# Kernel tuning notes

Measured on AMD Instinct MI355X. Metric: run time of the kernel, lower is better.

## Reference

```python
import jax, jax.numpy as jnp
import numpy as np

N = 80000        # nodes
E = 1280000      # edges
NG = 8           # graphs (segment ids)
F_IN = 3
NC = 20
BN_EPS = 1e-3    # keras BatchNormalization default epsilon


def setup_inputs() -> dict:
    key = jax.random.key(0)
    ks = jax.random.split(key, 16)
    inp = {}
    inp['x'] = jax.random.normal(ks[0], (N, F_IN), dtype=jnp.float32)
    inp['edge_w'] = jax.random.uniform(ks[1], (E,), dtype=jnp.float32)
    inp['src'] = jax.random.randint(ks[2], (E,), 0, N, dtype=jnp.int32)
    inp['dst'] = jax.random.randint(ks[3], (E,), 0, N, dtype=jnp.int32)
    inp['ids'] = jnp.sort(jax.random.randint(ks[4], (N,), 0, NG, dtype=jnp.int32))
    def w(k, fi, fo):
        return jax.random.normal(k, (fi, fo), dtype=jnp.float32) * (1.0 / np.sqrt(fi))
    inp['W1'] = w(ks[5], F_IN, 32); inp['b1'] = jnp.zeros((32,), jnp.float32)
    inp['W2'] = w(ks[6], 32, 32);   inp['b2'] = jnp.zeros((32,), jnp.float32)
    inp['g1'] = jnp.ones((32,), jnp.float32); inp['be1'] = jnp.zeros((32,), jnp.float32)
    inp['m1'] = jax.random.normal(ks[7], (32,), dtype=jnp.float32) * 0.1
    inp['v1'] = jax.random.uniform(ks[8], (32,), dtype=jnp.float32) + 0.5
    inp['W3'] = w(ks[9], 32, 64);   inp['b3'] = jnp.zeros((64,), jnp.float32)
    inp['W4'] = w(ks[10], 64, 64);  inp['b4'] = jnp.zeros((64,), jnp.float32)
    inp['g2'] = jnp.ones((64,), jnp.float32); inp['be2'] = jnp.zeros((64,), jnp.float32)
    inp['m2'] = jax.random.normal(ks[11], (64,), dtype=jnp.float32) * 0.1
    inp['v2'] = jax.random.uniform(ks[12], (64,), dtype=jnp.float32) + 0.5
    inp['W5'] = w(ks[13], 64, NC);  inp['b5'] = jnp.zeros((NC,), jnp.float32)
    return inp


def _gcn(x, W, b, src, dst, ew):
    # Spektral GCNConv: A_norm @ (X W) + b, with A given as edge list (src->dst).
    h = x @ W                                      # [N, Fo] dense transform first (cheaper)
    msg = h[src] * ew[:, None]                     # gather + scale  [E, Fo]
    agg = jax.ops.segment_sum(msg, dst, num_segments=N)  # scatter-add [N, Fo]
    return agg + b


def _bn(x, g, be, m, v):
    # inference-mode BatchNormalization
    return (x - m) * (g * jax.lax.rsqrt(v + BN_EPS)) + be


def _pool(x, ids):
    # per-graph global max pooling, broadcast back to nodes
    mx = jax.ops.segment_max(x, ids, num_segments=NG)   # [NG, F]
    return mx[ids]                                       # [N, F]


def reference(x, edge_w, src, dst, ids,
              W1, b1, W2, b2, g1, be1, m1, v1,
              W3, b3, W4, b4, g2, be2, m2, v2,
              W5, b5):
    h = jax.nn.relu(_gcn(x, W1, b1, src, dst, edge_w))
    h = jax.nn.relu(_gcn(h, W2, b2, src, dst, edge_w))
    h = _bn(h, g1, be1, m1, v1)
    h = _pool(h, ids)
    h = jax.nn.relu(_gcn(h, W3, b3, src, dst, edge_w))
    h = jax.nn.relu(_gcn(h, W4, b4, src, dst, edge_w))
    h = _bn(h, g2, be2, m2, v2)
    h = _pool(h, ids)
    # dropout is identity in inference
    out = jax.nn.softmax(_gcn(h, W5, b5, src, dst, edge_w), axis=-1)
    return out
```

## Files before the change

kernel.cpp:

```cpp
#include <hip/hip_runtime.h>

#define NN 80000
#define NE 1280000
#define NGR 8
#define BN_EPS 1e-3f
#define NBF 625
#define GB 1280
#define CHK 1000

typedef unsigned short ushort;
typedef __attribute__((ext_vector_type(8))) short bf16x8;
typedef __attribute__((ext_vector_type(4))) float f32x4;

__device__ __forceinline__ unsigned enc_f(float f) {
    unsigned b = __float_as_uint(f);
    return (f >= 0.f) ? (b | 0x80000000u) : ~b;
}
__device__ __forceinline__ float dec_f(unsigned u) {
    return (u & 0x80000000u) ? __uint_as_float(u & 0x7FFFFFFFu) : __uint_as_float(~u);
}
__device__ __forceinline__ ushort f2bf(float f) {
    unsigned u = __float_as_uint(f);
    unsigned r = u + 0x7FFFu + ((u >> 16) & 1u);
    return (ushort)(r >> 16);
}
__device__ __forceinline__ void fma8(float* acc, const ushort* p, float w) {
    uint4 q = *(const uint4*)p;
    acc[0] += w * __uint_as_float((q.x & 0xFFFFu) << 16);
    acc[1] += w * __uint_as_float(q.x & 0xFFFF0000u);
    acc[2] += w * __uint_as_float((q.y & 0xFFFFu) << 16);
    acc[3] += w * __uint_as_float(q.y & 0xFFFF0000u);
    acc[4] += w * __uint_as_float((q.z & 0xFFFFu) << 16);
    acc[5] += w * __uint_as_float(q.z & 0xFFFF0000u);
    acc[6] += w * __uint_as_float((q.w & 0xFFFFu) << 16);
    acc[7] += w * __uint_as_float(q.w & 0xFFFF0000u);
}

__global__ __launch_bounds__(256) void k_bhist(const int* __restrict__ dst,
                                               int* __restrict__ hcnt) {
    __shared__ int lh[NBF];
    for (int i = threadIdx.x; i < NBF; i += 256) lh[i] = 0;
    __syncthreads();
    int e0 = blockIdx.x * CHK;
    for (int e = e0 + threadIdx.x; e < e0 + CHK; e += 256)
        atomicAdd(&lh[dst[e] >> 7], 1);
    __syncthreads();
    int* row = hcnt + (size_t)blockIdx.x * NBF;
    for (int i = threadIdx.x; i < NBF; i += 256) row[i] = lh[i];
}

__global__ __launch_bounds__(256) void k_bbase1(int* __restrict__ hcnt,
                                                int* __restrict__ tot) {
    __shared__ int sm[256];
    int bin = blockIdx.x, t = threadIdx.x;
    int v[5];
    int s = 0;
    #pragma unroll
    for (int j = 0; j < 5; ++j) {
        v[j] = hcnt[(size_t)(t * 5 + j) * NBF + bin];
        s += v[j];
    }
    sm[t] = s;
    __syncthreads();
    #pragma unroll
    for (int off = 1; off < 256; off <<= 1) {
        int u = (t >= off) ? sm[t - off] : 0;
        __syncthreads();
        sm[t] += u;
        __syncthreads();
    }
    int run = sm[t] - s;
    if (t == 255) tot[bin] = sm[255];
    #pragma unroll
    for (int j = 0; j < 5; ++j) {
        hcnt[(size_t)(t * 5 + j) * NBF + bin] = run;
        run += v[j];
    }
}

__global__ __launch_bounds__(1024) void k_bbase2(const int* __restrict__ tot,
                                                 int* __restrict__ bo) {
    __shared__ int sm[1024];
    int t = threadIdx.x;
    int v = (t < NBF) ? tot[t] : 0;
    sm[t] = v;
    __syncthreads();
    #pragma unroll
    for (int off = 1; off < 1024; off <<= 1) {
        int u = (t >= off) ? sm[t - off] : 0;
        __syncthreads();
        sm[t] += u;
        __syncthreads();
    }
    if (t < NBF) bo[t] = sm[t] - v;
    if (t == 0) bo[NBF] = NE;
}

__global__ __launch_bounds__(256) void k_bfill(const int* __restrict__ src,
                                               const int* __restrict__ dst,
                                               const float* __restrict__ ew,
                                               const int* __restrict__ ids,
                                               const int* __restrict__ hcnt,
                                               const int* __restrict__ bo,
                                               int2* __restrict__ cB) {
    __shared__ int lcur[NBF];
    const int* row = hcnt + (size_t)blockIdx.x * NBF;
    for (int i = threadIdx.x; i < NBF; i += 256) lcur[i] = row[i] + bo[i];
    __syncthreads();
    int e0 = blockIdx.x * CHK;
    for (int e = e0 + threadIdx.x; e < e0 + CHK; e += 256) {
        int d = dst[e];
        int s = src[e];
        int pos = atomicAdd(&lcur[d >> 7], 1);
        cB[pos] = make_int2(s | (ids[s] << 17) | ((d & 127) << 20),
                            __float_as_int(ew[e]));
    }
}

__global__ __launch_bounds__(512) void k_insort(const int* __restrict__ bo,
                                                const int2* __restrict__ cB,
                                                int* __restrict__ rp,
                                                int2* __restrict__ cE) {
    __shared__ int lc[128];
    __shared__ int loff[128];
    __shared__ int sm[512];
    int bin = blockIdx.x, t = threadIdx.x;
    int s0 = bo[bin], s1 = bo[bin + 1];
    if (t < 128) lc[t] = 0;
    __syncthreads();
    for (int i = s0 + t; i < s1; i += 512)
        atomicAdd(&lc[(cB[i].x >> 20) & 127], 1);
    __syncthreads();
    int v = (t < 128) ? lc[t] : 0;
    sm[t] = v;
    __syncthreads();
    #pragma unroll
    for (int off = 1; off < 128; off <<= 1) {
        int u = (t >= off && t < 128) ? sm[t - off] : 0;
        __syncthreads();
        if (t < 128) sm[t] += u;
        __syncthreads();
    }
    if (t < 128) {
        loff[t] = sm[t] - v;
        rp[bin * 128 + t] = s0 + loff[t];
        lc[t] = 0;
    }
    if (bin == NBF - 1 && t == 0) rp[NN] = NE;
    __syncthreads();
    for (int i = s0 + t; i < s1; i += 512) {
        int2 a = cB[i];
        int dlow = (a.x >> 20) & 127;
        int pos = s0 + loff[dlow] + atomicAdd(&lc[dlow], 1);
        cE[pos] = make_int2((a.x & 0x1FFFF) | (((a.x >> 17) & 7) << 24), a.y);
    }
}

__global__ __launch_bounds__(256) void k_wprep(const float* __restrict__ W2,
                                               const float* __restrict__ W4,
                                               ushort* __restrict__ W2t,
                                               ushort* __restrict__ W4t) {
    int t = threadIdx.x;
    for (int i = t; i < 32 * 32; i += 256) {
        int f = i >> 5, k = i & 31;
        W2t[i] = f2bf(W2[k * 32 + f]);
    }
    for (int i = t; i < 64 * 64; i += 256) {
        int f = i >> 6, k = i & 63;
        W4t[i] = f2bf(W4[k * 64 + f]);
    }
}

__global__ __launch_bounds__(256) void k_gSX(const float* __restrict__ x,
                                             const int* __restrict__ rp,
                                             const int2* __restrict__ cE,
                                             float* __restrict__ S,
                                             float* __restrict__ AX) {
    int n = blockIdx.x * 256 + threadIdx.x;
    if (n >= NN) return;
    int e0 = rp[n], e1 = rp[n + 1];
    float sv[8] = {0, 0, 0, 0, 0, 0, 0, 0};
    float ax0 = 0.f, ax1 = 0.f, ax2 = 0.f;
    for (int i = e0; i < e1; ++i) {
        int2 a = cE[i];
        float w = __int_as_float(a.y);
        int s = a.x & 0xFFFFFF;
        int gg = a.x >> 24;
        #pragma unroll
        for (int g = 0; g < 8; ++g) sv[g] += (gg == g) ? w : 0.f;
        const float* xp = x + s * 3;
        ax0 += w * xp[0]; ax1 += w * xp[1]; ax2 += w * xp[2];
    }
    float4* Sp = (float4*)(S + n * 8);
    Sp[0] = make_float4(sv[0], sv[1], sv[2], sv[3]);
    Sp[1] = make_float4(sv[4], sv[5], sv[6], sv[7]);
    *(float4*)(AX + n * 4) = make_float4(ax0, ax1, ax2, 0.f);
}

__global__ __launch_bounds__(256) void k_l12m(const float* __restrict__ AX,
                                              const float* __restrict__ W1,
                                              const float* __restrict__ b1,
                                              const ushort* __restrict__ W2t,
                                              ushort* __restrict__ T) {
    __shared__ ushort h1s[64 * 40];
    int t = threadIdx.x;
    int nb = blockIdx.x * 64;
    {
        int f = t & 31, rr = t >> 5;
        float w0 = W1[f], w1 = W1[32 + f], w2 = W1[64 + f], bb = b1[f];
        #pragma unroll
        for (int i = 0; i < 8; ++i) {
            int n = rr + i * 8;
            float4 ax = *(const float4*)(AX + (nb + n) * 4);
            float acc = bb + ax.x * w0 + ax.y * w1 + ax.z * w2;
            h1s[n * 40 + f] = f2bf(fmaxf(acc, 0.f));
        }
    }
    __syncthreads();
    int lane = t & 63, wave = t >> 6;
    int quad = lane >> 4, col = lane & 15;
    int mtile = wave;
    bf16x8 a = *(const bf16x8*)(h1s + (mtile * 16 + col) * 40 + quad * 8);
    #pragma unroll
    for (int ntile = 0; ntile < 2; ++ntile) {
        bf16x8 b = *(const bf16x8*)(W2t + (ntile * 16 + col) * 32 + quad * 8);
        f32x4 acc = {0.f, 0.f, 0.f, 0.f};
        acc = __builtin_amdgcn_mfma_f32_16x16x32_bf16(a, b, acc, 0, 0, 0);
        #pragma unroll
        for (int r = 0; r < 4; ++r) {
            int node = nb + mtile * 16 + quad * 4 + r;
            T[node * 32 + ntile * 16 + col] = f2bf(acc[r]);
        }
    }
}

__global__ __launch_bounds__(256) void k_l34m(const float* __restrict__ S,
                                              const float* __restrict__ HW3,
                                              const float* __restrict__ b3,
                                              const ushort* __restrict__ W4t,
                                              ushort* __restrict__ T) {
    __shared__ ushort h3s[64 * 72];
    int t = threadIdx.x;
    int nb = blockIdx.x * 64;
    {
        int f = t & 63, rr = t >> 6;
        float hwc[8];
        #pragma unroll
        for (int g = 0; g < 8; ++g) hwc[g] = HW3[g * 64 + f];
        float bb = b3[f];
        #pragma unroll
        for (int i = 0; i < 16; ++i) {
            int n = rr + i * 4;
            const float4* sp = (const float4*)(S + (size_t)(nb + n) * 8);
            float4 s0 = sp[0], s1 = sp[1];
            float acc = bb + s0.x * hwc[0] + s0.y * hwc[1] + s0.z * hwc[2] +
                        s0.w * hwc[3] + s1.x * hwc[4] + s1.y * hwc[5] +
                        s1.z * hwc[6] + s1.w * hwc[7];
            h3s[n * 72 + f] = f2bf(fmaxf(acc, 0.f));
        }
    }
    __syncthreads();
    int lane = t & 63, wave = t >> 6;
    int quad = lane >> 4, col = lane & 15;
    int mtile = wave;
    bf16x8 a0 = *(const bf16x8*)(h3s + (mtile * 16 + col) * 72 + quad * 8);
    bf16x8 a1 = *(const bf16x8*)(h3s + (mtile * 16 + col) * 72 + 32 + quad * 8);
    #pragma unroll
    for (int ntile = 0; ntile < 4; ++ntile) {
        bf16x8 b0 = *(const bf16x8*)(W4t + (ntile * 16 + col) * 64 + quad * 8);
        bf16x8 b1v = *(const bf16x8*)(W4t + (ntile * 16 + col) * 64 + 32 + quad * 8);
        f32x4 acc = {0.f, 0.f, 0.f, 0.f};
        acc = __builtin_amdgcn_mfma_f32_16x16x32_bf16(a0, b0, acc, 0, 0, 0);
        acc = __builtin_amdgcn_mfma_f32_16x16x32_bf16(a1, b1v, acc, 0, 0, 0);
        #pragma unroll
        for (int r = 0; r < 4; ++r) {
            int node = nb + mtile * 16 + quad * 4 + r;
            T[node * 64 + ntile * 16 + col] = f2bf(acc[r]);
        }
    }
}

template <int LOGF>
__global__ __launch_bounds__(256) void k_gpool(const ushort* __restrict__ th,
                                               const int* __restrict__ rp,
                                               const int2* __restrict__ cE,
                                               const int* __restrict__ ids,
                                               const float* __restrict__ b,
                                               const float* __restrict__ g,
                                               const float* __restrict__ be,
                                               const float* __restrict__ m,
                                               const float* __restrict__ v,
                                               unsigned* __restrict__ mxe) {
    const int F = 1 << LOGF;
    const int CPN = F >> 3;
    const int NPB = 256 / CPN;
    __shared__ unsigned lmx[NGR * F];
    for (int i = threadIdx.x; i < NGR * F; i += 256) lmx[i] = 0u;
    __syncthreads();
    int c = threadIdx.x & (CPN - 1);
    int n = blockIdx.x * NPB + (threadIdx.x >> (LOGF - 3));
    if (n < NN) {
        int e0 = rp[n], e1 = rp[n + 1];
        float acc[8] = {0, 0, 0, 0, 0, 0, 0, 0};
        float acc2[8] = {0, 0, 0, 0, 0, 0, 0, 0};
        int i = e0;
        for (; i + 2 <= e1; i += 2) {
            int2 a0 = cE[i], a1 = cE[i + 1];
            const ushort* p0 = th + (((size_t)(a0.x & 0xFFFFFF)) << LOGF) + (c << 3);
            const ushort* p1 = th + (((size_t)(a1.x & 0xFFFFFF)) << LOGF) + (c << 3);
            fma8(acc, p0, __int_as_float(a0.y));
            fma8(acc2, p1, __int_as_float(a1.y));
        }
        if (i < e1) {
            int2 a0 = cE[i];
            fma8(acc, th + (((size_t)(a0.x & 0xFFFFFF)) << LOGF) + (c << 3),
                 __int_as_float(a0.y));
        }
        int gg = ids[n];
        #pragma unroll
        for (int j = 0; j < 8; ++j) {
            int f = (c << 3) + j;
            float scale = g[f] * rsqrtf(v[f] + BN_EPS);
            float h = fmaxf(acc[j] + acc2[j] + b[f], 0.f);
            float val = (h - m[f]) * scale + be[f];
            atomicMax(&lmx[gg * F + f], enc_f(val));
        }
    }
    __syncthreads();
    for (int i = threadIdx.x; i < NGR * F; i += 256) {
        unsigned u = lmx[i];
        if (u) atomicMax(&mxe[i], u);
    }
}

__global__ __launch_bounds__(512) void k_dechw3(const unsigned* __restrict__ mxe,
                                                const float* __restrict__ W,
                                                float* __restrict__ HW) {
    __shared__ float smx[256];
    int t = threadIdx.x;
    if (t < 256) smx[t] = mxe[t] ? dec_f(mxe[t]) : 0.f;
    __syncthreads();
    int g = t >> 6, f = t & 63;
    float acc = 0.f;
    #pragma unroll
    for (int k = 0; k < 32; ++k) acc += smx[g * 32 + k] * W[k * 64 + f];
    HW[t] = acc;
}

__global__ __launch_bounds__(512) void k_dechw5(const unsigned* __restrict__ mxe,
                                                const float* __restrict__ W,
                                                float* __restrict__ HW) {
    __shared__ float smx[512];
    int t = threadIdx.x;
    smx[t] = mxe[t] ? dec_f(mxe[t]) : 0.f;
    __syncthreads();
    if (t >= 160) return;
    int g = t / 20, c = t % 20;
    float acc = 0.f;
    #pragma unroll
    for (int k = 0; k < 64; ++k) acc += smx[g * 64 + k] * W[k * 20 + c];
    HW[t] = acc;
}

__global__ __launch_bounds__(256) void k_out(const float* __restrict__ S,
                                             const float* __restrict__ HW5,
                                             const float* __restrict__ b5,
                                             float* __restrict__ out) {
    __shared__ float hw[160];
    __shared__ float bb[20];
    int t = threadIdx.x;
    if (t < 160) hw[t] = HW5[t];
    if (t < 20) bb[t] = b5[t];
    __syncthreads();
    int n = blockIdx.x * 256 + t;
    if (n >= NN) return;
    const float4* sp = (const float4*)(S + n * 8);
    float4 s0 = sp[0], s1 = sp[1];
    float sv[8] = {s0.x, s0.y, s0.z, s0.w, s1.x, s1.y, s1.z, s1.w};
    float pre[20];
    #pragma unroll
    for (int c = 0; c < 20; ++c) {
        float acc = bb[c];
        #pragma unroll
        for (int g = 0; g < 8; ++g) acc += sv[g] * hw[g * 20 + c];
        pre[c] = acc;
    }
    float mx = pre[0];
    #pragma unroll
    for (int c = 1; c < 20; ++c) mx = fmaxf(mx, pre[c]);
    float sum = 0.f;
    #pragma unroll
    for (int c = 0; c < 20; ++c) { pre[c] = __expf(pre[c] - mx); sum += pre[c]; }
    float inv = 1.f / sum;
    #pragma unroll
    for (int c = 0; c < 20; ++c) out[n * 20 + c] = pre[c] * inv;
}

extern "C" void kernel_launch(void* const* d_in, const int* in_sizes, int n_in,
                              void* d_out, int out_size, void* d_ws, size_t ws_size,
                              hipStream_t stream) {
    const float* x   = (const float*)d_in[0];
    const float* ew  = (const float*)d_in[1];
    const int*   src = (const int*)d_in[2];
    const int*   dst = (const int*)d_in[3];
    const int*   ids = (const int*)d_in[4];
    const float* W1 = (const float*)d_in[5];  const float* b1 = (const float*)d_in[6];
    const float* W2 = (const float*)d_in[7];  const float* b2 = (const float*)d_in[8];
    const float* g1 = (const float*)d_in[9];  const float* be1 = (const float*)d_in[10];
    const float* m1 = (const float*)d_in[11]; const float* v1 = (const float*)d_in[12];
    const float* W3 = (const float*)d_in[13]; const float* b3 = (const float*)d_in[14];
    const float* W4 = (const float*)d_in[15]; const float* b4 = (const float*)d_in[16];
    const float* g2 = (const float*)d_in[17]; const float* be2 = (const float*)d_in[18];
    const float* m2 = (const float*)d_in[19]; const float* v2 = (const float*)d_in[20];
    const float* W5 = (const float*)d_in[21]; const float* b5 = (const float*)d_in[22];
    float* out = (float*)d_out;

    char* p = (char*)d_ws;
    float*  S    = (float*)p;  p += (size_t)NN * 8 * 4;
    ushort* T    = (ushort*)p; p += (size_t)NN * 64 * 2;
    float*  AX   = (float*)p;  p += (size_t)NN * 4 * 4;
    int*    rp   = (int*)p;    p += (size_t)(NN + 16) * 4;
    int*    hcnt = (int*)p;    p += (size_t)GB * NBF * 4;
    int*    tot  = (int*)p;    p += 1024 * 4;
    int*    bo   = (int*)p;    p += 1024 * 4;
    int2*   cB   = (int2*)p;   p += (size_t)NE * 8;
    int2*   cE   = (int2*)p;   p += (size_t)NE * 8;
    unsigned* MXE1 = (unsigned*)p; p += 256 * 4;
    unsigned* MXE2 = (unsigned*)p; p += 512 * 4;
    float*  HW3  = (float*)p;  p += 512 * 4;
    float*  HW5  = (float*)p;  p += 256 * 4;
    ushort* W2t  = (ushort*)p; p += 1024 * 2;
    ushort* W4t  = (ushort*)p; p += 4096 * 2;

    const int BS = 256;
    const int gN = (NN + BS - 1) / BS;

    hipMemsetAsync(MXE1, 0, 768 * 4, stream);
    hipLaunchKernelGGL(k_wprep, dim3(1), dim3(BS), 0, stream, W2, W4, W2t, W4t);
    hipLaunchKernelGGL(k_bhist, dim3(GB), dim3(BS), 0, stream, dst, hcnt);
    hipLaunchKernelGGL(k_bbase1, dim3(NBF), dim3(BS), 0, stream, hcnt, tot);
    hipLaunchKernelGGL(k_bbase2, dim3(1), dim3(1024), 0, stream, tot, bo);
    hipLaunchKernelGGL(k_bfill, dim3(GB), dim3(BS), 0, stream, src, dst, ew, ids, hcnt, bo, cB);
    hipLaunchKernelGGL(k_insort, dim3(NBF), dim3(512), 0, stream, bo, cB, rp, cE);

    hipLaunchKernelGGL(k_gSX, dim3(gN), dim3(BS), 0, stream, x, rp, cE, S, AX);

    hipLaunchKernelGGL(k_l12m, dim3(NN / 64), dim3(BS), 0, stream, AX, W1, b1, W2t, T);
    hipLaunchKernelGGL(k_gpool<5>, dim3(NN / 64), dim3(BS), 0, stream, T, rp, cE, ids, b2, g1, be1, m1, v1, MXE1);

    hipLaunchKernelGGL(k_dechw3, dim3(1), dim3(512), 0, stream, MXE1, W3, HW3);
    hipLaunchKernelGGL(k_l34m, dim3(NN / 64), dim3(BS), 0, stream, S, HW3, b3, W4t, T);
    hipLaunchKernelGGL(k_gpool<6>, dim3(NN / 32), dim3(BS), 0, stream, T, rp, cE, ids, b4, g2, be2, m2, v2, MXE2);

    hipLaunchKernelGGL(k_dechw5, dim3(1), dim3(512), 0, stream, MXE2, W5, HW5);
    hipLaunchKernelGGL(k_out, dim3(gN), dim3(BS), 0, stream, S, HW5, b5, out);
}
```

Measured before the change: 274.1 us.

## Fuse small prep kernels into neighbors and widen gather unrolling

Folds the weight-transpose prep into the bin-base scan kernel, fuses the per-node S/AX gather into the insertion-sort kernel (4 threads per node with shuffle reductions), and recomputes the pooled-max times W3/W5 products redundantly inside each block of the consuming kernels. This removes four kernel launches and the extra pass reading cE for S/AX. The gpool gather loop is unrolled to four independent accumulators to raise memory-level parallelism. In exchange, every block of k_l34m and k_out repeats a small matvec.

```diff
diff --git a/kernel.cpp b/kernel.cpp
--- a/kernel.cpp
+++ b/kernel.cpp
@@ -78,8 +78,12 @@
     }
 }
 
-__global__ __launch_bounds__(1024) void k_bbase2(const int* __restrict__ tot,
-                                                 int* __restrict__ bo) {
+__global__ __launch_bounds__(1024) void k_bbase2w(const int* __restrict__ tot,
+                                                  int* __restrict__ bo,
+                                                  const float* __restrict__ W2,
+                                                  const float* __restrict__ W4,
+                                                  ushort* __restrict__ W2t,
+                                                  ushort* __restrict__ W4t) {
     __shared__ int sm[1024];
     int t = threadIdx.x;
     int v = (t < NBF) ? tot[t] : 0;
@@ -94,6 +98,16 @@
     }
     if (t < NBF) bo[t] = sm[t] - v;
     if (t == 0) bo[NBF] = NE;
+    {
+        int f = t >> 5, k = t & 31;
+        W2t[t] = f2bf(W2[k * 32 + f]);
+    }
+    #pragma unroll
+    for (int j = 0; j < 4; ++j) {
+        int i = t + j * 1024;
+        int f = i >> 6, k = i & 63;
+        W4t[i] = f2bf(W4[k * 64 + f]);
+    }
 }
 
 __global__ __launch_bounds__(256) void k_bfill(const int* __restrict__ src,
@@ -119,8 +133,11 @@
 
 __global__ __launch_bounds__(512) void k_insort(const int* __restrict__ bo,
                                                 const int2* __restrict__ cB,
+                                                const float* __restrict__ x,
                                                 int* __restrict__ rp,
-                                                int2* __restrict__ cE) {
+                                                int2* __restrict__ cE,
+                                                float* __restrict__ S,
+                                                float* __restrict__ AX) {
     __shared__ int lc[128];
     __shared__ int loff[128];
     __shared__ int sm[512];
@@ -154,34 +171,13 @@
         int pos = s0 + loff[dlow] + atomicAdd(&lc[dlow], 1);
         cE[pos] = make_int2((a.x & 0x1FFFF) | (((a.x >> 17) & 7) << 24), a.y);
     }
-}
-
-__global__ __launch_bounds__(256) void k_wprep(const float* __restrict__ W2,
-                                               const float* __restrict__ W4,
-                                               ushort* __restrict__ W2t,
-                                               ushort* __restrict__ W4t) {
-    int t = threadIdx.x;
-    for (int i = t; i < 32 * 32; i += 256) {
-        int f = i >> 5, k = i & 31;
-        W2t[i] = f2bf(W2[k * 32 + f]);
-    }
-    for (int i = t; i < 64 * 64; i += 256) {
-        int f = i >> 6, k = i & 63;
-        W4t[i] = f2bf(W4[k * 64 + f]);
-    }
-}
-
-__global__ __launch_bounds__(256) void k_gSX(const float* __restrict__ x,
-                                             const int* __restrict__ rp,
-                                             const int2* __restrict__ cE,
-                                             float* __restrict__ S,
-                                             float* __restrict__ AX) {
-    int n = blockIdx.x * 256 + threadIdx.x;
-    if (n >= NN) return;
-    int e0 = rp[n], e1 = rp[n + 1];
+    __syncthreads();
+    int n = t >> 2, q = t & 3;
+    int ne0 = s0 + loff[n];
+    int ne1 = ne0 + lc[n];
     float sv[8] = {0, 0, 0, 0, 0, 0, 0, 0};
     float ax0 = 0.f, ax1 = 0.f, ax2 = 0.f;
-    for (int i = e0; i < e1; ++i) {
+    for (int i = ne0 + q; i < ne1; i += 4) {
         int2 a = cE[i];
         float w = __int_as_float(a.y);
         int s = a.x & 0xFFFFFF;
@@ -191,10 +187,21 @@
         const float* xp = x + s * 3;
         ax0 += w * xp[0]; ax1 += w * xp[1]; ax2 += w * xp[2];
     }
-    float4* Sp = (float4*)(S + n * 8);
-    Sp[0] = make_float4(sv[0], sv[1], sv[2], sv[3]);
-    Sp[1] = make_float4(sv[4], sv[5], sv[6], sv[7]);
-    *(float4*)(AX + n * 4) = make_float4(ax0, ax1, ax2, 0.f);
+    #pragma unroll
+    for (int g = 0; g < 8; ++g) {
+        sv[g] += __shfl_xor(sv[g], 1);
+        sv[g] += __shfl_xor(sv[g], 2);
+    }
+    ax0 += __shfl_xor(ax0, 1); ax0 += __shfl_xor(ax0, 2);
+    ax1 += __shfl_xor(ax1, 1); ax1 += __shfl_xor(ax1, 2);
+    ax2 += __shfl_xor(ax2, 1); ax2 += __shfl_xor(ax2, 2);
+    if (q == 0) {
+        int node = bin * 128 + n;
+        float4* Sp = (float4*)(S + (size_t)node * 8);
+        Sp[0] = make_float4(sv[0], sv[1], sv[2], sv[3]);
+        Sp[1] = make_float4(sv[4], sv[5], sv[6], sv[7]);
+        *(float4*)(AX + (size_t)node * 4) = make_float4(ax0, ax1, ax2, 0.f);
+    }
 }
 
 __global__ __launch_bounds__(256) void k_l12m(const float* __restrict__ AX,
@@ -235,18 +242,35 @@
 }
 
 __global__ __launch_bounds__(256) void k_l34m(const float* __restrict__ S,
-                                              const float* __restrict__ HW3,
+                                              const unsigned* __restrict__ mxe,
+                                              const float* __restrict__ W3,
                                               const float* __restrict__ b3,
                                               const ushort* __restrict__ W4t,
                                               ushort* __restrict__ T) {
+    __shared__ float smxs[256];
+    __shared__ float HW3s[512];
     __shared__ ushort h3s[64 * 72];
     int t = threadIdx.x;
     int nb = blockIdx.x * 64;
+    smxs[t] = mxe[t] ? dec_f(mxe[t]) : 0.f;
+    __syncthreads();
+    {
+        #pragma unroll
+        for (int j = 0; j < 2; ++j) {
+            int i = t + j * 256;
+            int g = i >> 6, f = i & 63;
+            float acc = 0.f;
+            #pragma unroll
+            for (int k = 0; k < 32; ++k) acc += smxs[g * 32 + k] * W3[k * 64 + f];
+            HW3s[i] = acc;
+        }
+    }
+    __syncthreads();
     {
         int f = t & 63, rr = t >> 6;
         float hwc[8];
         #pragma unroll
-        for (int g = 0; g < 8; ++g) hwc[g] = HW3[g * 64 + f];
+        for (int g = 0; g < 8; ++g) hwc[g] = HW3s[g * 64 + f];
         float bb = b3[f];
         #pragma unroll
         for (int i = 0; i < 16; ++i) {
@@ -301,27 +325,28 @@
     int n = blockIdx.x * NPB + (threadIdx.x >> (LOGF - 3));
     if (n < NN) {
         int e0 = rp[n], e1 = rp[n + 1];
-        float acc[8] = {0, 0, 0, 0, 0, 0, 0, 0};
-        float acc2[8] = {0, 0, 0, 0, 0, 0, 0, 0};
+        float a0[8] = {0, 0, 0, 0, 0, 0, 0, 0};
+        float a1[8] = {0, 0, 0, 0, 0, 0, 0, 0};
+        float a2[8] = {0, 0, 0, 0, 0, 0, 0, 0};
+        float a3[8] = {0, 0, 0, 0, 0, 0, 0, 0};
         int i = e0;
-        for (; i + 2 <= e1; i += 2) {
-            int2 a0 = cE[i], a1 = cE[i + 1];
-            const ushort* p0 = th + (((size_t)(a0.x & 0xFFFFFF)) << LOGF) + (c << 3);
-            const ushort* p1 = th + (((size_t)(a1.x & 0xFFFFFF)) << LOGF) + (c << 3);
-            fma8(acc, p0, __int_as_float(a0.y));
-            fma8(acc2, p1, __int_as_float(a1.y));
-        }
-        if (i < e1) {
-            int2 a0 = cE[i];
-            fma8(acc, th + (((size_t)(a0.x & 0xFFFFFF)) << LOGF) + (c << 3),
-                 __int_as_float(a0.y));
+        for (; i + 4 <= e1; i += 4) {
+            int2 q0 = cE[i], q1 = cE[i + 1], q2 = cE[i + 2], q3 = cE[i + 3];
+            fma8(a0, th + (((size_t)(q0.x & 0xFFFFFF)) << LOGF) + (c << 3), __int_as_float(q0.y));
+            fma8(a1, th + (((size_t)(q1.x & 0xFFFFFF)) << LOGF) + (c << 3), __int_as_float(q1.y));
+            fma8(a2, th + (((size_t)(q2.x & 0xFFFFFF)) << LOGF) + (c << 3), __int_as_float(q2.y));
+            fma8(a3, th + (((size_t)(q3.x & 0xFFFFFF)) << LOGF) + (c << 3), __int_as_float(q3.y));
+        }
+        for (; i < e1; ++i) {
+            int2 q0 = cE[i];
+            fma8(a0, th + (((size_t)(q0.x & 0xFFFFFF)) << LOGF) + (c << 3), __int_as_float(q0.y));
         }
         int gg = ids[n];
         #pragma unroll
         for (int j = 0; j < 8; ++j) {
             int f = (c << 3) + j;
             float scale = g[f] * rsqrtf(v[f] + BN_EPS);
-            float h = fmaxf(acc[j] + acc2[j] + b[f], 0.f);
+            float h = fmaxf((a0[j] + a1[j]) + (a2[j] + a3[j]) + b[f], 0.f);
             float val = (h - m[f]) * scale + be[f];
             atomicMax(&lmx[gg * F + f], enc_f(val));
         }
@@ -333,48 +358,30 @@
     }
 }
 
-__global__ __launch_bounds__(512) void k_dechw3(const unsigned* __restrict__ mxe,
-                                                const float* __restrict__ W,
-                                                float* __restrict__ HW) {
-    __shared__ float smx[256];
-    int t = threadIdx.x;
-    if (t < 256) smx[t] = mxe[t] ? dec_f(mxe[t]) : 0.f;
-    __syncthreads();
-    int g = t >> 6, f = t & 63;
-    float acc = 0.f;
-    #pragma unroll
-    for (int k = 0; k < 32; ++k) acc += smx[g * 32 + k] * W[k * 64 + f];
-    HW[t] = acc;
-}
-
-__global__ __launch_bounds__(512) void k_dechw5(const unsigned* __restrict__ mxe,
-                                                const float* __restrict__ W,
-                                                float* __restrict__ HW) {
-    __shared__ float smx[512];
-    int t = threadIdx.x;
-    smx[t] = mxe[t] ? dec_f(mxe[t]) : 0.f;
-    __syncthreads();
-    if (t >= 160) return;
-    int g = t / 20, c = t % 20;
-    float acc = 0.f;
-    #pragma unroll
-    for (int k = 0; k < 64; ++k) acc += smx[g * 64 + k] * W[k * 20 + c];
-    HW[t] = acc;
-}
-
 __global__ __launch_bounds__(256) void k_out(const float* __restrict__ S,
-                                             const float* __restrict__ HW5,
+                                             const unsigned* __restrict__ mxe,
+                                             const float* __restrict__ W5,
                                              const float* __restrict__ b5,
                                              float* __restrict__ out) {
+    __shared__ float smxs[512];
     __shared__ float hw[160];
     __shared__ float bb[20];
     int t = threadIdx.x;
-    if (t < 160) hw[t] = HW5[t];
+    smxs[t] = mxe[t] ? dec_f(mxe[t]) : 0.f;
+    smxs[t + 256] = mxe[t + 256] ? dec_f(mxe[t + 256]) : 0.f;
     if (t < 20) bb[t] = b5[t];
+    __syncthreads();
+    if (t < 160) {
+        int g = t / 20, c = t % 20;
+        float acc = 0.f;
+        #pragma unroll
+        for (int k = 0; k < 64; ++k) acc += smxs[g * 64 + k] * W5[k * 20 + c];
+        hw[t] = acc;
+    }
     __syncthreads();
     int n = blockIdx.x * 256 + t;
     if (n >= NN) return;
-    const float4* sp = (const float4*)(S + n * 8);
+    const float4* sp = (const float4*)(S + (size_t)n * 8);
     float4 s0 = sp[0], s1 = sp[1];
     float sv[8] = {s0.x, s0.y, s0.z, s0.w, s1.x, s1.y, s1.z, s1.w};
     float pre[20];
@@ -427,8 +434,6 @@
     int2*   cE   = (int2*)p;   p += (size_t)NE * 8;
     unsigned* MXE1 = (unsigned*)p; p += 256 * 4;
     unsigned* MXE2 = (unsigned*)p; p += 512 * 4;
-    float*  HW3  = (float*)p;  p += 512 * 4;
-    float*  HW5  = (float*)p;  p += 256 * 4;
     ushort* W2t  = (ushort*)p; p += 1024 * 2;
     ushort* W4t  = (ushort*)p; p += 4096 * 2;
 
@@ -436,22 +441,17 @@
     const int gN = (NN + BS - 1) / BS;
 
     hipMemsetAsync(MXE1, 0, 768 * 4, stream);
-    hipLaunchKernelGGL(k_wprep, dim3(1), dim3(BS), 0, stream, W2, W4, W2t, W4t);
     hipLaunchKernelGGL(k_bhist, dim3(GB), dim3(BS), 0, stream, dst, hcnt);
     hipLaunchKernelGGL(k_bbase1, dim3(NBF), dim3(BS), 0, stream, hcnt, tot);
-    hipLaunchKernelGGL(k_bbase2, dim3(1), dim3(1024), 0, stream, tot, bo);
+    hipLaunchKernelGGL(k_bbase2w, dim3(1), dim3(1024), 0, stream, tot, bo, W2, W4, W2t, W4t);
     hipLaunchKernelGGL(k_bfill, dim3(GB), dim3(BS), 0, stream, src, dst, ew, ids, hcnt, bo, cB);
-    hipLaunchKernelGGL(k_insort, dim3(NBF), dim3(512), 0, stream, bo, cB, rp, cE);
-
-    hipLaunchKernelGGL(k_gSX, dim3(gN), dim3(BS), 0, stream, x, rp, cE, S, AX);
+    hipLaunchKernelGGL(k_insort, dim3(NBF), dim3(512), 0, stream, bo, cB, x, rp, cE, S, AX);
 
     hipLaunchKernelGGL(k_l12m, dim3(NN / 64), dim3(BS), 0, stream, AX, W1, b1, W2t, T);
     hipLaunchKernelGGL(k_gpool<5>, dim3(NN / 64), dim3(BS), 0, stream, T, rp, cE, ids, b2, g1, be1, m1, v1, MXE1);
 
-    hipLaunchKernelGGL(k_dechw3, dim3(1), dim3(512), 0, stream, MXE1, W3, HW3);
-    hipLaunchKernelGGL(k_l34m, dim3(NN / 64), dim3(BS), 0, stream, S, HW3, b3, W4t, T);
+    hipLaunchKernelGGL(k_l34m, dim3(NN / 64), dim3(BS), 0, stream, S, MXE1, W3, b3, W4t, T);
     hipLaunchKernelGGL(k_gpool<6>, dim3(NN / 32), dim3(BS), 0, stream, T, rp, cE, ids, b4, g2, be2, m2, v2, MXE2);
 
-    hipLaunchKernelGGL(k_dechw5, dim3(1), dim3(512), 0, stream, MXE2, W5, HW5);
-    hipLaunchKernelGGL(k_out, dim3(gN), dim3(BS), 0, stream, S, HW5, b5, out);
-}
+    hipLaunchKernelGGL(k_out, dim3(gN), dim3(BS), 0, stream, S, MXE2, W5, b5, out);
+}
```

After: 259.0 us. 5.5% less time.
